# Kernel optimization log

Hardware: AMD Instinct MI355X
Metric: run time of the kernel (lower is better)

## Reference

```python
import jax, jax.numpy as jnp
import numpy as np

BATCH, SEQ, H, P, HID, CHUNK = 2, 2048, 32, 64, 2048, 256
NORM_EPS = 1e-5


def setup_inputs() -> dict:
    key = jax.random.key(0)
    ks = jax.random.split(key, 10)
    f = lambda k, sh, sc=1.0: jax.random.normal(k, sh, jnp.float32) * sc
    return {
        "hidden_states_ab": f(ks[0], (BATCH, SEQ, HID), 0.02),
        "hidden_states_g": f(ks[1], (BATCH, SEQ, HID), 0.02),
        "q_states": f(ks[2], (BATCH, SEQ, H, P)),
        "k_states": f(ks[3], (BATCH, SEQ, H, P)),
        "v_states": f(ks[4], (BATCH, SEQ, H, P)),
        "dt_w": f(ks[5], (HID, H), 0.02),
        "dt_b": jnp.zeros((H,), jnp.float32),
        "g_w": f(ks[6], (HID, H), 0.02),
        "g_b": jnp.zeros((H,), jnp.float32),
        "A_log": jnp.log(jnp.arange(1, H + 1, dtype=jnp.float32)),
        "dt_bias": jnp.ones((H,), jnp.float32),
        "norm_weight": jnp.ones((H * P,), jnp.float32),
        "o_w": f(ks[7], (H, P, P), 0.02),
        "o_b": jnp.zeros((H, P), jnp.float32),
    }


def _l2norm(x, eps=1e-12):
    # torch F.normalize(p=2, dim=-1): x / max(||x||, eps)
    n = jnp.sqrt(jnp.sum(x * x, axis=-1, keepdims=True))
    return x / jnp.maximum(n, eps)


def _ssd(x, dt, A, Bm, Cm, chunk):
    # x: (b,s,h,p)  dt: (b,s,h) post-softplus  A: (h,)  Bm/Cm: (b,s,h,n)
    b, s, h, p = x.shape
    n = Bm.shape[-1]
    c = s // chunk
    rs = lambda t: t.reshape(b, c, chunk, *t.shape[2:])
    x, dt, Bm, Cm = rs(x), rs(dt), rs(Bm), rs(Cm)
    a = dt * A                         # (b,c,L,h) log-decay increments
    cum = jnp.cumsum(a, axis=2)        # (b,c,L,h)
    cumT = jnp.swapaxes(cum, 2, 3)     # (b,c,h,L)
    # intra-chunk (quadratic, causal) part
    diff = cumT[..., :, None] - cumT[..., None, :]          # (b,c,h,L,L)
    mask = jnp.tril(jnp.ones((chunk, chunk), bool))
    decay = jnp.exp(jnp.where(mask, diff, -jnp.inf))
    CB = jnp.einsum('bclhn,bcshn->bchls', Cm, Bm)
    scores = CB * decay * jnp.swapaxes(dt, 2, 3)[:, :, :, None, :]
    y = jnp.einsum('bchls,bcshp->bclhp', scores, x)
    # per-chunk states
    decay_last = jnp.exp(cumT[..., -1:] - cumT)             # (b,c,h,L)
    w = jnp.swapaxes(decay_last, 2, 3) * dt                 # (b,c,L,h)
    states = jnp.einsum('bclh,bclhn,bclhp->bchpn', w, Bm, x)
    # inter-chunk recurrence over c chunks
    chunk_decay = jnp.exp(cumT[..., -1])                    # (b,c,h)
    def step(Hs, inp):
        cd, st = inp
        return cd[..., None, None] * Hs + st, Hs
    H_last, H_prev = jax.lax.scan(
        step, jnp.zeros((b, h, p, n), x.dtype),
        (jnp.moveaxis(chunk_decay, 1, 0), jnp.moveaxis(states, 1, 0)))
    H_prev = jnp.moveaxis(H_prev, 0, 1)                     # (b,c,h,p,n)
    y = y + jnp.einsum('bclhn,bclh,bchpn->bclhp', Cm, jnp.exp(cum), H_prev)
    return y.reshape(b, s, h, p), H_last


def reference(hidden_states_ab, hidden_states_g, q_states, k_states, v_states,
              dt_w, dt_b, g_w, g_b, A_log, dt_bias, norm_weight, o_w, o_b):
    b, s, h, p = v_states.shape
    Cm = _l2norm(q_states)
    Bm = _l2norm(k_states)
    # dt_proj bias + mamba dt_bias, then softplus (dt_softplus=True)
    dt = jax.nn.softplus(hidden_states_ab @ dt_w + dt_b + dt_bias)   # (b,s,h)
    A = -jnp.exp(A_log)
    y, ssm_state = _ssd(v_states, dt, A, Bm, Cm, CHUNK)
    # gate: g_proj then repeat_interleave(head_dim) on last dim
    gate = jnp.repeat(hidden_states_g @ g_w + g_b, p, axis=-1)       # (b,s,h*p)
    # RMSNormGated, norm_before_gate=False: normalize(x * silu(z)) * weight
    y = y.reshape(b, s, h * p) * jax.nn.silu(gate)
    y = y * jax.lax.rsqrt(jnp.mean(y * y, axis=-1, keepdims=True) + NORM_EPS)
    y = y * norm_weight
    # GroupLinear o_proj: per-head (p -> p) linear
    out = jnp.einsum('bshp,hpq->bshq', y.reshape(b, s, h, p), o_w) + o_b
    return out.reshape(b, s, h * p)
```

## Files before the change

### kernel.cpp

```cpp
#include <hip/hip_runtime.h>
#include <math.h>

#define BATCH 2
#define SEQ   2048
#define NH    32
#define HID   2048
#define CHUNK 256
#define NCH   8
#define NBCH  (BATCH*NCH*NH)
#define PST   72
#define BK    256
#define APST  264
#define KSPLIT 4
#define KSEG  (HID / KSPLIT)

typedef __attribute__((ext_vector_type(4))) float f32x4;
typedef __attribute__((ext_vector_type(8))) short bf16x8;
typedef unsigned int uint;
typedef unsigned short ushort;

__device__ __forceinline__ float softplusf(float x) {
    return x > 20.f ? x : log1pf(expf(x));
}

__device__ __forceinline__ short f2bf(float f) {
    union { float f; uint u; } v; v.f = f;
    uint r = v.u + 0x7FFF + ((v.u >> 16) & 1);
    return (short)(r >> 16);
}
__device__ __forceinline__ float bf2f(ushort s) {
    union { uint u; float f; } v; v.u = ((uint)s) << 16; return v.f;
}
__device__ __forceinline__ uint packbf2(float lo, float hi) {
    return (uint)(ushort)f2bf(lo) | ((uint)(ushort)f2bf(hi) << 16);
}

struct BF8 { union { bf16x8 v; short s[8]; }; };

__device__ __forceinline__ bf16x8 load_cvt8(const float* p, float scale) {
    float4 a = *(const float4*)p;
    float4 b = *(const float4*)(p + 4);
    BF8 r;
    r.s[0]=f2bf(a.x*scale); r.s[1]=f2bf(a.y*scale); r.s[2]=f2bf(a.z*scale); r.s[3]=f2bf(a.w*scale);
    r.s[4]=f2bf(b.x*scale); r.s[5]=f2bf(b.y*scale); r.s[6]=f2bf(b.z*scale); r.s[7]=f2bf(b.w*scale);
    return r.v;
}

#define MFMA(a,b,c) __builtin_amdgcn_mfma_f32_16x16x32_bf16((a),(b),(c),0,0,0)

__global__ __launch_bounds__(256) void k_proj(
    const float* __restrict__ hs_ab, const float* __restrict__ hs_g,
    const float* __restrict__ dt_w, const float* __restrict__ g_w,
    float* __restrict__ part)
{
    __shared__ short As[32 * APST];
    __shared__ short Bs[32 * APST];
    int blk = blockIdx.x;
    int ksp = blk >> 8;
    int rem = blk & 255;
    int which = rem >> 7;
    int rt = rem & 127;
    int r0 = rt * 32;
    const float* Am = which ? hs_g : hs_ab;
    const float* W  = which ? g_w  : dt_w;
    int t = threadIdx.x;
    int w = t >> 6, lane = t & 63, quad = lane >> 4, l16 = lane & 15;
    int mh = w & 1, nh = w >> 1;

    f32x4 acc = (f32x4){0.f, 0.f, 0.f, 0.f};

    for (int kc = ksp * KSEG; kc < ksp * KSEG + KSEG; kc += BK) {
        __syncthreads();
        {
            int row = t >> 3, k0 = (t & 7) * 32;
            const float* src = Am + (size_t)(r0 + row) * HID + kc + k0;
            uint* dst = (uint*)(As + row * APST + k0);
            #pragma unroll
            for (int i = 0; i < 4; ++i) {
                float4 a = *(const float4*)(src + i * 8);
                float4 b = *(const float4*)(src + i * 8 + 4);
                dst[i*4+0] = packbf2(a.x, a.y); dst[i*4+1] = packbf2(a.z, a.w);
                dst[i*4+2] = packbf2(b.x, b.y); dst[i*4+3] = packbf2(b.z, b.w);
            }
        }
        if (t < 128) {
            int k2 = t * 2;
            const float* w0 = W + (size_t)(kc + k2) * NH;
            const float* w1 = w0 + NH;
            #pragma unroll
            for (int n = 0; n < 32; n += 4) {
                float4 a = *(const float4*)(w0 + n);
                float4 b = *(const float4*)(w1 + n);
                *((uint*)(Bs + (n+0) * APST + k2)) = packbf2(a.x, b.x);
                *((uint*)(Bs + (n+1) * APST + k2)) = packbf2(a.y, b.y);
                *((uint*)(Bs + (n+2) * APST + k2)) = packbf2(a.z, b.z);
                *((uint*)(Bs + (n+3) * APST + k2)) = packbf2(a.w, b.w);
            }
        }
        __syncthreads();
        #pragma unroll
        for (int ks = 0; ks < BK / 32; ++ks) {
            bf16x8 af = *(const bf16x8*)(As + (mh*16 + l16) * APST + ks*32 + quad*8);
            bf16x8 bf = *(const bf16x8*)(Bs + (nh*16 + l16) * APST + ks*32 + quad*8);
            acc = MFMA(af, bf, acc);
        }
    }

    int n = nh * 16 + l16;
    int Rb = r0 + mh * 16 + quad * 4;
    float* pd = part + ((size_t)(which * KSPLIT + ksp) * 4096 + Rb) * 32 + n;
    #pragma unroll
    for (int r = 0; r < 4; ++r)
        pd[r * 32] = acc[r];
}

__global__ __launch_bounds__(256) void k_proj_fin(
    const float* __restrict__ part,
    const float* __restrict__ dt_b, const float* __restrict__ g_b,
    const float* __restrict__ dt_bias,
    float* __restrict__ dt_out, float* __restrict__ g_out)
{
    int id = blockIdx.x * 256 + threadIdx.x;
    int which = id >> 17;
    int rid = id & 131071;
    int n = rid & 31;
    const float* p = part + (size_t)which * (KSPLIT * 131072) + rid;
    float s = p[0] + p[131072] + p[262144] + p[393216];
    if (which == 0)
        dt_out[rid] = softplusf(s + dt_b[n] + dt_bias[n]);
    else
        g_out[rid] = s + g_b[n];
}

__global__ __launch_bounds__(256) void k_norms(
    const float* __restrict__ q, const float* __restrict__ k,
    float* __restrict__ invC, float* __restrict__ invB)
{
    int t = threadIdx.x;
    int lane = t & 63;
    size_t row = (size_t)blockIdx.x * 4 + (t >> 6);
    float qv = q[row * 64 + lane];
    float kv = k[row * 64 + lane];
    float sq = qv * qv, sk = kv * kv;
    #pragma unroll
    for (int off = 32; off > 0; off >>= 1) {
        sq += __shfl_down(sq, off);
        sk += __shfl_down(sk, off);
    }
    if (lane == 0) {
        invC[row] = 1.f / fmaxf(sqrtf(sq), 1e-12f);
        invB[row] = 1.f / fmaxf(sqrtf(sk), 1e-12f);
    }
}

__global__ __launch_bounds__(256) void k_cumsum(
    const float* __restrict__ dt, const float* __restrict__ A_log,
    float* __restrict__ cumc, float* __restrict__ wvc,
    float* __restrict__ dtc, float* __restrict__ cd)
{
    __shared__ float sC[256];
    int bch = blockIdx.x;
    int h = bch & 31, c = (bch >> 5) & 7, b = bch >> 8;
    int t = threadIdx.x;
    size_t row = ((size_t)b * SEQ + c * CHUNK + t) * NH + h;
    float dt_l = dt[row];
    float A = -expf(A_log[h]);
    sC[t] = dt_l * A;
    __syncthreads();
    for (int off = 1; off < 256; off <<= 1) {
        float v = (t >= off) ? sC[t - off] : 0.f;
        __syncthreads();
        sC[t] += v;
        __syncthreads();
    }
    float cum = sC[t], cl = sC[255];
    size_t o = (size_t)bch * CHUNK + t;
    cumc[o] = cum;
    wvc[o] = expf(cl - cum) * dt_l;
    dtc[o] = dt_l;
    if (t == 255) cd[bch] = expf(cl);
}

__global__ __launch_bounds__(256) void k_states(
    const float* __restrict__ kst, const float* __restrict__ vst,
    const float* __restrict__ invB, const float* __restrict__ wvc,
    float* __restrict__ sp)
{
    __shared__ float kS[64 * 64];
    __shared__ float xS[64 * 64];
    int blk = blockIdx.x;
    int half = blk & 1, bch = blk >> 1;
    int h = bch & 31, c = (bch >> 5) & 7, b = bch >> 8;
    int t = threadIdx.x;
    size_t rowbase = (size_t)b * SEQ + c * CHUNK + half * 128;
    int pg = (t & 15) * 4, ng = (t >> 4) * 4;
    float acc[4][4];
    #pragma unroll
    for (int i = 0; i < 4; ++i)
        #pragma unroll
        for (int j = 0; j < 4; ++j) acc[i][j] = 0.f;

    for (int tt = 0; tt < 2; ++tt) {
        int r0 = t >> 4;
        int c4 = (t & 15) * 4;
        #pragma unroll
        for (int i = 0; i < 4; ++i) {
            int row = r0 + i * 16;
            size_t grow = (rowbase + tt * 64 + row) * NH + h;
            float w  = wvc[(size_t)bch * CHUNK + half * 128 + tt * 64 + row];
            float ib = invB[grow];
            float4 kv = *(const float4*)(kst + grow * 64 + c4);
            float4 xv = *(const float4*)(vst + grow * 64 + c4);
            *(float4*)(kS + row * 64 + c4) =
                make_float4(kv.x * ib, kv.y * ib, kv.z * ib, kv.w * ib);
            *(float4*)(xS + row * 64 + c4) =
                make_float4(xv.x * w, xv.y * w, xv.z * w, xv.w * w);
        }
        __syncthreads();
        for (int ll = 0; ll < 64; ++ll) {
            float4 x4 = *(const float4*)(xS + ll * 64 + pg);
            float4 k4 = *(const float4*)(kS + ll * 64 + ng);
            acc[0][0] += x4.x * k4.x; acc[0][1] += x4.x * k4.y;
            acc[0][2] += x4.x * k4.z; acc[0][3] += x4.x * k4.w;
            acc[1][0] += x4.y * k4.x; acc[1][1] += x4.y * k4.y;
            acc[1][2] += x4.y * k4.z; acc[1][3] += x4.y * k4.w;
            acc[2][0] += x4.z * k4.x; acc[2][1] += x4.z * k4.y;
            acc[2][2] += x4.z * k4.z; acc[2][3] += x4.z * k4.w;
            acc[3][0] += x4.w * k4.x; acc[3][1] += x4.w * k4.y;
            acc[3][2] += x4.w * k4.z; acc[3][3] += x4.w * k4.w;
        }
        __syncthreads();
    }
    size_t obase = (size_t)blk * 4096;
    #pragma unroll
    for (int i = 0; i < 4; ++i)
        *(float4*)(sp + obase + (pg + i) * 64 + ng) =
            make_float4(acc[i][0], acc[i][1], acc[i][2], acc[i][3]);
}

__global__ __launch_bounds__(256) void k_scan(
    const float* __restrict__ sp, const float* __restrict__ cd,
    float* __restrict__ Hp)
{
    size_t id = (size_t)blockIdx.x * 256 + threadIdx.x;
    size_t bh = id >> 12, pn = id & 4095;
    size_t b = bh >> 5, h = bh & 31;
    float carry = 0.f;
    for (int c = 0; c < NCH; ++c) {
        size_t bch = (b * NCH + c) * NH + h;
        float st = sp[(bch * 2) * 4096 + pn] + sp[(bch * 2 + 1) * 4096 + pn];
        Hp[bch * 4096 + pn] = carry;
        carry = cd[bch] * carry + st;
    }
}

__global__ __launch_bounds__(256, 2) void k_intra(
    const float* __restrict__ qst, const float* __restrict__ kst,
    const float* __restrict__ vst,
    const float* __restrict__ invC, const float* __restrict__ invB,
    const float* __restrict__ cumc, const float* __restrict__ dtc,
    const float* __restrict__ Hp,
    short* __restrict__ ygb)
{
    __shared__ short B_s[64 * PST];
    __shared__ short XT_s[64 * PST];
    __shared__ short P_s[4 * 32 * PST];
    __shared__ float sCum[256];
    __shared__ float sDt[256];

    int bch = blockIdx.x;
    int h = bch & 31, c = (bch >> 5) & 7, b = bch >> 8;
    int t = threadIdx.x;
    int w = t >> 6, lane = t & 63;
    int quad = lane >> 4, l16 = lane & 15;
    size_t rowbase = (size_t)b * SEQ + c * CHUNK;

    sCum[t] = cumc[(size_t)bch * CHUNK + t];
    sDt[t]  = dtc[(size_t)bch * CHUNK + t];
    __syncthreads();

    bf16x8 cf[2][2][2];
    #pragma unroll
    for (int is = 0; is < 2; ++is) {
        int strip = is ? (7 - w) : w;
        #pragma unroll
        for (int lt = 0; lt < 2; ++lt) {
            int l = strip * 32 + lt * 16 + l16;
            size_t grow = (rowbase + l) * NH + h;
            float ic = invC[grow];
            const float* qp = qst + grow * 64 + quad * 8;
            cf[is][lt][0] = load_cvt8(qp, ic);
            cf[is][lt][1] = load_cvt8(qp + 32, ic);
        }
    }

    f32x4 acc[2][2][4];
    #pragma unroll
    for (int is = 0; is < 2; ++is)
        #pragma unroll
        for (int lt = 0; lt < 2; ++lt)
            #pragma unroll
            for (int pt = 0; pt < 4; ++pt)
                acc[is][lt][pt] = (f32x4){0.f, 0.f, 0.f, 0.f};

    {
        bf16x8 hf[4][2];
        #pragma unroll
        for (int pt = 0; pt < 4; ++pt) {
            const float* hp = Hp + (size_t)bch * 4096 + (pt * 16 + l16) * 64 + quad * 8;
            hf[pt][0] = load_cvt8(hp, 1.f);
            hf[pt][1] = load_cvt8(hp + 32, 1.f);
        }
        #pragma unroll
        for (int is = 0; is < 2; ++is)
            #pragma unroll
            for (int lt = 0; lt < 2; ++lt)
                #pragma unroll
                for (int pt = 0; pt < 4; ++pt) {
                    acc[is][lt][pt] = MFMA(cf[is][lt][0], hf[pt][0], acc[is][lt][pt]);
                    acc[is][lt][pt] = MFMA(cf[is][lt][1], hf[pt][1], acc[is][lt][pt]);
                }
    }
    #pragma unroll
    for (int is = 0; is < 2; ++is) {
        int strip = is ? (7 - w) : w;
        #pragma unroll
        for (int lt = 0; lt < 2; ++lt) {
            float e[4];
            #pragma unroll
            for (int r = 0; r < 4; ++r)
                e[r] = __expf(sCum[strip * 32 + lt * 16 + quad * 4 + r]);
            #pragma unroll
            for (int pt = 0; pt < 4; ++pt)
                #pragma unroll
                for (int r = 0; r < 4; ++r)
                    acc[is][lt][pt][r] *= e[r];
        }
    }

    short* Pw = P_s + w * 32 * PST;

    for (int st = 0; st < 4; ++st) {
        __syncthreads();
        {
            int ss = t >> 2, q4 = (t & 3) * 16;
            size_t grow = (rowbase + st * 64 + ss) * NH + h;
            float ib = invB[grow];
            const float4* kp = (const float4*)(kst + grow * 64 + q4);
            float4 v0 = kp[0], v1 = kp[1], v2 = kp[2], v3 = kp[3];
            uint u[8];
            u[0] = packbf2(v0.x * ib, v0.y * ib); u[1] = packbf2(v0.z * ib, v0.w * ib);
            u[2] = packbf2(v1.x * ib, v1.y * ib); u[3] = packbf2(v1.z * ib, v1.w * ib);
            u[4] = packbf2(v2.x * ib, v2.y * ib); u[5] = packbf2(v2.z * ib, v2.w * ib);
            u[6] = packbf2(v3.x * ib, v3.y * ib); u[7] = packbf2(v3.z * ib, v3.w * ib);
            uint* dst = (uint*)(B_s + ss * PST + q4);
            *(uint4*)dst = make_uint4(u[0], u[1], u[2], u[3]);
            *(uint4*)(dst + 4) = make_uint4(u[4], u[5], u[6], u[7]);
        }
        {
            int ss2 = t & 31, qh = t >> 5;
            int p0 = qh * 8;
            size_t g0 = (rowbase + st * 64 + 2 * ss2) * NH + h;
            size_t g1 = g0 + NH;
            float dt0 = sDt[st * 64 + 2 * ss2];
            float dt1 = sDt[st * 64 + 2 * ss2 + 1];
            float4 a0 = *(const float4*)(vst + g0 * 64 + p0);
            float4 a1 = *(const float4*)(vst + g0 * 64 + p0 + 4);
            float4 b0 = *(const float4*)(vst + g1 * 64 + p0);
            float4 b1 = *(const float4*)(vst + g1 * 64 + p0 + 4);
            float x0[8] = {a0.x, a0.y, a0.z, a0.w, a1.x, a1.y, a1.z, a1.w};
            float x1[8] = {b0.x, b0.y, b0.z, b0.w, b1.x, b1.y, b1.z, b1.w};
            uint* xt = (uint*)XT_s;
            #pragma unroll
            for (int i = 0; i < 8; ++i)
                xt[(p0 + i) * (PST / 2) + ss2] = packbf2(x0[i] * dt0, x1[i] * dt1);
        }
        __syncthreads();

        bf16x8 xf[4][2];
        #pragma unroll
        for (int pt = 0; pt < 4; ++pt) {
            #pragma unroll
            for (int ks = 0; ks < 2; ++ks)
                xf[pt][ks] = *(const bf16x8*)(XT_s + (pt * 16 + l16) * PST + ks * 32 + quad * 8);
        }

        #pragma unroll
        for (int is = 0; is < 2; ++is) {
            int strip = is ? (7 - w) : w;
            int L0 = strip * 32;
            if (L0 + 31 < st * 64) continue;

            #pragma unroll
            for (int lt = 0; lt < 2; ++lt) {
                int Lt = L0 + lt * 16;
                float cl = sCum[Lt + l16];
                int lrow = lt * 16 + l16;
                #pragma unroll
                for (int mt = 0; mt < 4; ++mt) {
                    int S0 = st * 64 + mt * 16;
                    uint* pdst = (uint*)(Pw + lrow * PST + mt * 16 + quad * 4);
                    if (S0 > Lt + 15) {
                        *(uint2*)pdst = make_uint2(0u, 0u);
                        continue;
                    }
                    f32x4 sa = (f32x4){0.f, 0.f, 0.f, 0.f};
                    bf16x8 af0 = *(const bf16x8*)(B_s + (mt * 16 + l16) * PST + quad * 8);
                    bf16x8 af1 = *(const bf16x8*)(B_s + (mt * 16 + l16) * PST + 32 + quad * 8);
                    sa = MFMA(af0, cf[is][lt][0], sa);
                    sa = MFMA(af1, cf[is][lt][1], sa);
                    float vals[4];
                    #pragma unroll
                    for (int r = 0; r < 4; ++r) {
                        int s = S0 + quad * 4 + r;
                        float v = sa[r] * __expf(cl - sCum[s]);
                        vals[r] = (Lt + l16 >= s) ? v : 0.f;
                    }
                    *(uint2*)pdst = make_uint2(packbf2(vals[0], vals[1]),
                                               packbf2(vals[2], vals[3]));
                }
            }
            #pragma unroll
            for (int lt = 0; lt < 2; ++lt) {
                int Lmax = L0 + lt * 16 + 15;
                #pragma unroll
                for (int ks = 0; ks < 2; ++ks) {
                    if (st * 64 + ks * 32 > Lmax) continue;
                    bf16x8 af = *(const bf16x8*)(Pw + (lt * 16 + l16) * PST + ks * 32 + quad * 8);
                    #pragma unroll
                    for (int pt = 0; pt < 4; ++pt)
                        acc[is][lt][pt] = MFMA(af, xf[pt][ks], acc[is][lt][pt]);
                }
            }
        }
    }

    #pragma unroll
    for (int is = 0; is < 2; ++is) {
        int strip = is ? (7 - w) : w;
        #pragma unroll
        for (int lt = 0; lt < 2; ++lt)
            #pragma unroll
            for (int pt = 0; pt < 4; ++pt)
                #pragma unroll
                for (int r = 0; r < 4; ++r) {
                    int l = strip * 32 + lt * 16 + quad * 4 + r;
                    int p = pt * 16 + l16;
                    ygb[((rowbase + l) * NH + h) * 64 + p] = f2bf(acc[is][lt][pt][r]);
                }
    }
}

__global__ __launch_bounds__(256) void k_gate(
    const short* __restrict__ ygb, const float* __restrict__ g_ws,
    const float* __restrict__ norm_w, short* __restrict__ ygn)
{
    __shared__ float sil[32];
    __shared__ float red[256];
    int r = blockIdx.x;
    int t = threadIdx.x;
    if (t < 32) {
        float g = g_ws[(size_t)r * 32 + t];
        sil[t] = g / (1.f + expf(-g));
    }
    __syncthreads();
    uint4 u = *(const uint4*)(ygb + (size_t)r * 2048 + t * 8);
    float s = sil[t >> 3];
    float v[8];
    v[0] = bf2f(u.x & 0xFFFF) * s; v[1] = bf2f(u.x >> 16) * s;
    v[2] = bf2f(u.y & 0xFFFF) * s; v[3] = bf2f(u.y >> 16) * s;
    v[4] = bf2f(u.z & 0xFFFF) * s; v[5] = bf2f(u.z >> 16) * s;
    v[6] = bf2f(u.w & 0xFFFF) * s; v[7] = bf2f(u.w >> 16) * s;
    float ssq = 0.f;
    #pragma unroll
    for (int i = 0; i < 8; ++i) ssq += v[i] * v[i];
    red[t] = ssq;
    __syncthreads();
    for (int off = 128; off > 0; off >>= 1) {
        if (t < off) red[t] += red[t + off];
        __syncthreads();
    }
    float scale = rsqrtf(red[0] / 2048.f + 1e-5f);
    const float* nw = norm_w + t * 8;
    uint4 o;
    o.x = packbf2(v[0] * scale * nw[0], v[1] * scale * nw[1]);
    o.y = packbf2(v[2] * scale * nw[2], v[3] * scale * nw[3]);
    o.z = packbf2(v[4] * scale * nw[4], v[5] * scale * nw[5]);
    o.w = packbf2(v[6] * scale * nw[6], v[7] * scale * nw[7]);
    *(uint4*)(ygn + (size_t)r * 2048 + t * 8) = o;
}

__global__ __launch_bounds__(256) void k_oproj(
    const short* __restrict__ ygn, const float* __restrict__ o_w,
    const float* __restrict__ o_b, float* __restrict__ out)
{
    __shared__ short wT[64 * PST];
    int blk = blockIdx.x;
    int h = blk & 31, rt = blk >> 5;
    int t = threadIdx.x;
    int w = t >> 6, lane = t & 63;
    int quad = lane >> 4, l16 = lane & 15;

    {
        int p = t >> 2, q4 = (t & 3) * 16;
        const float* wp = o_w + (size_t)h * 4096 + p * 64 + q4;
        float4 v0 = *(const float4*)wp, v1 = *(const float4*)(wp + 4);
        float4 v2 = *(const float4*)(wp + 8), v3 = *(const float4*)(wp + 12);
        float vv[16] = {v0.x,v0.y,v0.z,v0.w, v1.x,v1.y,v1.z,v1.w,
                        v2.x,v2.y,v2.z,v2.w, v3.x,v3.y,v3.z,v3.w};
        #pragma unroll
        for (int i = 0; i < 16; ++i)
            wT[(q4 + i) * PST + p] = f2bf(vv[i]);
    }
    __syncthreads();

    bf16x8 bfr[4][2];
    #pragma unroll
    for (int nt = 0; nt < 4; ++nt)
        #pragma unroll
        for (int ks = 0; ks < 2; ++ks)
            bfr[nt][ks] = *(const bf16x8*)(wT + (nt * 16 + l16) * PST + ks * 32 + quad * 8);

    int rowbase = rt * 256 + w * 64;
    f32x4 acc[4][4];
    #pragma unroll
    for (int nt = 0; nt < 4; ++nt) {
        float bv = o_b[h * 64 + nt * 16 + l16];
        #pragma unroll
        for (int mt = 0; mt < 4; ++mt)
            acc[mt][nt] = (f32x4){bv, bv, bv, bv};
    }
    #pragma unroll
    for (int ks = 0; ks < 2; ++ks) {
        #pragma unroll
        for (int mt = 0; mt < 4; ++mt) {
            int row = rowbase + mt * 16 + l16;
            bf16x8 af = *(const bf16x8*)(ygn + (size_t)row * 2048 + h * 64 + ks * 32 + quad * 8);
            #pragma unroll
            for (int nt = 0; nt < 4; ++nt)
                acc[mt][nt] = MFMA(af, bfr[nt][ks], acc[mt][nt]);
        }
    }
    #pragma unroll
    for (int mt = 0; mt < 4; ++mt)
        #pragma unroll
        for (int nt = 0; nt < 4; ++nt)
            #pragma unroll
            for (int r = 0; r < 4; ++r) {
                int row = rowbase + mt * 16 + quad * 4 + r;
                out[(size_t)row * 2048 + h * 64 + nt * 16 + l16] = acc[mt][nt][r];
            }
}

extern "C" void kernel_launch(void* const* d_in, const int* in_sizes, int n_in,
                              void* d_out, int out_size, void* d_ws, size_t ws_size,
                              hipStream_t stream) {
    const float* hs_ab   = (const float*)d_in[0];
    const float* hs_g    = (const float*)d_in[1];
    const float* qst     = (const float*)d_in[2];
    const float* kst     = (const float*)d_in[3];
    const float* vst     = (const float*)d_in[4];
    const float* dt_w    = (const float*)d_in[5];
    const float* dt_b    = (const float*)d_in[6];
    const float* g_w     = (const float*)d_in[7];
    const float* g_b     = (const float*)d_in[8];
    const float* A_log   = (const float*)d_in[9];
    const float* dt_bias = (const float*)d_in[10];
    const float* norm_w  = (const float*)d_in[11];
    const float* o_w     = (const float*)d_in[12];
    const float* o_b     = (const float*)d_in[13];
    float* out = (float*)d_out;

    float* ws = (float*)d_ws;
    size_t off = 0;
    float* part   = ws + off; off += (size_t)2 * KSPLIT * 4096 * 32;
    float* dt_ws  = ws + off; off += (size_t)BATCH * SEQ * NH;
    float* g_ws   = ws + off; off += (size_t)BATCH * SEQ * NH;
    float* invC   = ws + off; off += (size_t)BATCH * SEQ * NH;
    float* invB   = ws + off; off += (size_t)BATCH * SEQ * NH;
    float* cumc   = ws + off; off += (size_t)NBCH * CHUNK;
    float* wvc    = ws + off; off += (size_t)NBCH * CHUNK;
    float* dtc    = ws + off; off += (size_t)NBCH * CHUNK;
    float* cd_ws  = ws + off; off += (size_t)NBCH;
    float* sp     = ws + off; off += (size_t)NBCH * 2 * 4096;
    float* Hp     = ws + off; off += (size_t)NBCH * 4096;

    short* ygb = (short*)sp;
    short* ygn = (short*)sp + (size_t)BATCH * SEQ * NH * 64;

    k_proj<<<2 * KSPLIT * (BATCH * SEQ / 32), 256, 0, stream>>>(
        hs_ab, hs_g, dt_w, g_w, part);
    k_proj_fin<<<2 * BATCH * SEQ * NH / 256, 256, 0, stream>>>(
        part, dt_b, g_b, dt_bias, dt_ws, g_ws);
    k_norms<<<BATCH * SEQ * NH / 4, 256, 0, stream>>>(qst, kst, invC, invB);
    k_cumsum<<<NBCH, 256, 0, stream>>>(dt_ws, A_log, cumc, wvc, dtc, cd_ws);
    k_states<<<NBCH * 2, 256, 0, stream>>>(kst, vst, invB, wvc, sp);
    k_scan<<<BATCH * NH * 4096 / 256, 256, 0, stream>>>(sp, cd_ws, Hp);
    k_intra<<<NBCH, 256, 0, stream>>>(qst, kst, vst, invC, invB,
                                      cumc, dtc, Hp, ygb);
    k_gate<<<BATCH * SEQ, 256, 0, stream>>>(ygb, g_ws, norm_w, ygn);
    k_oproj<<<32 * (BATCH * SEQ / 256), 256, 0, stream>>>(ygn, o_w, o_b, out);
}
```

Before: 286.7 us.

## Fuse projection finish, l2 norms, gating and o_proj to cut kernel launches

```diff
diff --git a/kernel.cpp b/kernel.cpp
--- a/kernel.cpp
+++ b/kernel.cpp
@@ -46,16 +46,51 @@
     return r.v;
 }
 
+__device__ __forceinline__ bf16x8 cvt8(float4 a, float4 b, float s) {
+    BF8 r;
+    r.s[0]=f2bf(a.x*s); r.s[1]=f2bf(a.y*s); r.s[2]=f2bf(a.z*s); r.s[3]=f2bf(a.w*s);
+    r.s[4]=f2bf(b.x*s); r.s[5]=f2bf(b.y*s); r.s[6]=f2bf(b.z*s); r.s[7]=f2bf(b.w*s);
+    return r.v;
+}
+
 #define MFMA(a,b,c) __builtin_amdgcn_mfma_f32_16x16x32_bf16((a),(b),(c),0,0,0)
 
 __global__ __launch_bounds__(256) void k_proj(
     const float* __restrict__ hs_ab, const float* __restrict__ hs_g,
     const float* __restrict__ dt_w, const float* __restrict__ g_w,
-    float* __restrict__ part)
+    const float* __restrict__ o_w,  const float* __restrict__ norm_w,
+    float* __restrict__ part, short* __restrict__ nwWT)
 {
-    __shared__ short As[32 * APST];
-    __shared__ short Bs[32 * APST];
+    __shared__ __align__(16) short As[32 * APST];
+    __shared__ __align__(16) short Bs[32 * APST];
     int blk = blockIdx.x;
+    int t = threadIdx.x;
+
+    if (blk >= 2 * KSPLIT * 128) {
+        int h = blk - 2 * KSPLIT * 128;
+        float* tile = (float*)As;
+        {
+            int p = t >> 2, q0 = (t & 3) * 16;
+            const float* wp = o_w + (size_t)h * 4096 + p * 64 + q0;
+            #pragma unroll
+            for (int i = 0; i < 4; ++i)
+                *(float4*)(tile + p * 64 + q0 + i * 4) = *(const float4*)(wp + i * 4);
+        }
+        __syncthreads();
+        int q = t >> 2, p0 = (t & 3) * 16;
+        uint us[8];
+        #pragma unroll
+        for (int j = 0; j < 8; ++j) {
+            float lo = tile[(p0 + 2*j    ) * 64 + q] * norm_w[h * 64 + p0 + 2*j];
+            float hi = tile[(p0 + 2*j + 1) * 64 + q] * norm_w[h * 64 + p0 + 2*j + 1];
+            us[j] = packbf2(lo, hi);
+        }
+        uint* dst = (uint*)(nwWT + (size_t)h * 4096 + q * 64 + p0);
+        *(uint4*)dst       = make_uint4(us[0], us[1], us[2], us[3]);
+        *(uint4*)(dst + 4) = make_uint4(us[4], us[5], us[6], us[7]);
+        return;
+    }
+
     int ksp = blk >> 8;
     int rem = blk & 255;
     int which = rem >> 7;
@@ -63,7 +98,6 @@
     int r0 = rt * 32;
     const float* Am = which ? hs_g : hs_ab;
     const float* W  = which ? g_w  : dt_w;
-    int t = threadIdx.x;
     int w = t >> 6, lane = t & 63, quad = lane >> 4, l16 = lane & 15;
     int mh = w & 1, nh = w >> 1;
 
@@ -114,80 +148,48 @@
         pd[r * 32] = acc[r];
 }
 
-__global__ __launch_bounds__(256) void k_proj_fin(
-    const float* __restrict__ part,
-    const float* __restrict__ dt_b, const float* __restrict__ g_b,
-    const float* __restrict__ dt_bias,
-    float* __restrict__ dt_out, float* __restrict__ g_out)
-{
-    int id = blockIdx.x * 256 + threadIdx.x;
-    int which = id >> 17;
-    int rid = id & 131071;
-    int n = rid & 31;
-    const float* p = part + (size_t)which * (KSPLIT * 131072) + rid;
-    float s = p[0] + p[131072] + p[262144] + p[393216];
-    if (which == 0)
-        dt_out[rid] = softplusf(s + dt_b[n] + dt_bias[n]);
-    else
-        g_out[rid] = s + g_b[n];
-}
-
-__global__ __launch_bounds__(256) void k_norms(
-    const float* __restrict__ q, const float* __restrict__ k,
-    float* __restrict__ invC, float* __restrict__ invB)
-{
-    int t = threadIdx.x;
-    int lane = t & 63;
-    size_t row = (size_t)blockIdx.x * 4 + (t >> 6);
-    float qv = q[row * 64 + lane];
-    float kv = k[row * 64 + lane];
-    float sq = qv * qv, sk = kv * kv;
-    #pragma unroll
-    for (int off = 32; off > 0; off >>= 1) {
-        sq += __shfl_down(sq, off);
-        sk += __shfl_down(sk, off);
-    }
-    if (lane == 0) {
-        invC[row] = 1.f / fmaxf(sqrtf(sq), 1e-12f);
-        invB[row] = 1.f / fmaxf(sqrtf(sk), 1e-12f);
-    }
-}
-
 __global__ __launch_bounds__(256) void k_cumsum(
-    const float* __restrict__ dt, const float* __restrict__ A_log,
+    const float* __restrict__ part, const float* __restrict__ dt_b,
+    const float* __restrict__ dt_bias, const float* __restrict__ A_log,
     float* __restrict__ cumc, float* __restrict__ wvc,
     float* __restrict__ dtc, float* __restrict__ cd)
 {
-    __shared__ float sC[256];
+    __shared__ float wsum[4];
     int bch = blockIdx.x;
     int h = bch & 31, c = (bch >> 5) & 7, b = bch >> 8;
     int t = threadIdx.x;
-    size_t row = ((size_t)b * SEQ + c * CHUNK + t) * NH + h;
-    float dt_l = dt[row];
+    int w = t >> 6, lane = t & 63;
+    int rid = (b * SEQ + c * CHUNK + t) * 32 + h;
+    float s = part[rid] + part[131072 + rid] + part[262144 + rid] + part[393216 + rid];
+    float dt_l = softplusf(s + dt_b[h] + dt_bias[h]);
     float A = -expf(A_log[h]);
-    sC[t] = dt_l * A;
+    float v = dt_l * A;
+    #pragma unroll
+    for (int off = 1; off < 64; off <<= 1) {
+        float u = __shfl_up(v, off);
+        if (lane >= off) v += u;
+    }
+    if (lane == 63) wsum[w] = v;
     __syncthreads();
-    for (int off = 1; off < 256; off <<= 1) {
-        float v = (t >= off) ? sC[t - off] : 0.f;
-        __syncthreads();
-        sC[t] += v;
-        __syncthreads();
-    }
-    float cum = sC[t], cl = sC[255];
+    float pre = 0.f;
+    #pragma unroll
+    for (int i = 0; i < 3; ++i)
+        if (i < w) pre += wsum[i];
+    float cum = v + pre;
+    float tot = wsum[0] + wsum[1] + wsum[2] + wsum[3];
     size_t o = (size_t)bch * CHUNK + t;
     cumc[o] = cum;
-    wvc[o] = expf(cl - cum) * dt_l;
+    wvc[o] = expf(tot - cum) * dt_l;
     dtc[o] = dt_l;
-    if (t == 255) cd[bch] = expf(cl);
+    if (t == 255) cd[bch] = expf(tot);
 }
 
 __global__ __launch_bounds__(256) void k_states(
     const float* __restrict__ kst, const float* __restrict__ vst,
-    const float* __restrict__ invB, const float* __restrict__ wvc,
-    float* __restrict__ sp)
+    const float* __restrict__ wvc, float* __restrict__ sp)
 {
-    __shared__ float kS[64 * 64];
-    __shared__ float xS[64 * 64];
+    __shared__ __align__(16) float kS[64 * 64];
+    __shared__ __align__(16) float xS[64 * 64];
     int blk = blockIdx.x;
     int half = blk & 1, bch = blk >> 1;
     int h = bch & 31, c = (bch >> 5) & 7, b = bch >> 8;
@@ -207,14 +209,17 @@
         for (int i = 0; i < 4; ++i) {
             int row = r0 + i * 16;
             size_t grow = (rowbase + tt * 64 + row) * NH + h;
-            float w  = wvc[(size_t)bch * CHUNK + half * 128 + tt * 64 + row];
-            float ib = invB[grow];
+            float wv = wvc[(size_t)bch * CHUNK + half * 128 + tt * 64 + row];
             float4 kv = *(const float4*)(kst + grow * 64 + c4);
             float4 xv = *(const float4*)(vst + grow * 64 + c4);
+            float ssq = kv.x*kv.x + kv.y*kv.y + kv.z*kv.z + kv.w*kv.w;
+            ssq += __shfl_xor(ssq, 1); ssq += __shfl_xor(ssq, 2);
+            ssq += __shfl_xor(ssq, 4); ssq += __shfl_xor(ssq, 8);
+            float ib = 1.f / fmaxf(sqrtf(ssq), 1e-12f);
             *(float4*)(kS + row * 64 + c4) =
                 make_float4(kv.x * ib, kv.y * ib, kv.z * ib, kv.w * ib);
             *(float4*)(xS + row * 64 + c4) =
-                make_float4(xv.x * w, xv.y * w, xv.z * w, xv.w * w);
+                make_float4(xv.x * wv, xv.y * wv, xv.z * wv, xv.w * wv);
         }
         __syncthreads();
         for (int ll = 0; ll < 64; ++ll) {
@@ -257,14 +262,13 @@
 __global__ __launch_bounds__(256, 2) void k_intra(
     const float* __restrict__ qst, const float* __restrict__ kst,
     const float* __restrict__ vst,
-    const float* __restrict__ invC, const float* __restrict__ invB,
     const float* __restrict__ cumc, const float* __restrict__ dtc,
     const float* __restrict__ Hp,
     short* __restrict__ ygb)
 {
-    __shared__ short B_s[64 * PST];
-    __shared__ short XT_s[64 * PST];
-    __shared__ short P_s[4 * 32 * PST];
+    __shared__ __align__(16) short B_s[64 * PST];
+    __shared__ __align__(16) short XT_s[64 * PST];
+    __shared__ __align__(16) short P_s[4 * 32 * PST];
     __shared__ float sCum[256];
     __shared__ float sDt[256];
 
@@ -287,10 +291,20 @@
         for (int lt = 0; lt < 2; ++lt) {
             int l = strip * 32 + lt * 16 + l16;
             size_t grow = (rowbase + l) * NH + h;
-            float ic = invC[grow];
             const float* qp = qst + grow * 64 + quad * 8;
-            cf[is][lt][0] = load_cvt8(qp, ic);
-            cf[is][lt][1] = load_cvt8(qp + 32, ic);
+            float4 a  = *(const float4*)qp;
+            float4 bq = *(const float4*)(qp + 4);
+            float4 c2 = *(const float4*)(qp + 32);
+            float4 d  = *(const float4*)(qp + 36);
+            float ssq = a.x*a.x + a.y*a.y + a.z*a.z + a.w*a.w
+                      + bq.x*bq.x + bq.y*bq.y + bq.z*bq.z + bq.w*bq.w
+                      + c2.x*c2.x + c2.y*c2.y + c2.z*c2.z + c2.w*c2.w
+                      + d.x*d.x + d.y*d.y + d.z*d.z + d.w*d.w;
+            ssq += __shfl_xor(ssq, 16);
+            ssq += __shfl_xor(ssq, 32);
+            float ic = 1.f / fmaxf(sqrtf(ssq), 1e-12f);
+            cf[is][lt][0] = cvt8(a, bq, ic);
+            cf[is][lt][1] = cvt8(c2, d, ic);
         }
     }
 
@@ -345,9 +359,15 @@
         {
             int ss = t >> 2, q4 = (t & 3) * 16;
             size_t grow = (rowbase + st * 64 + ss) * NH + h;
-            float ib = invB[grow];
             const float4* kp = (const float4*)(kst + grow * 64 + q4);
             float4 v0 = kp[0], v1 = kp[1], v2 = kp[2], v3 = kp[3];
+            float ssq = v0.x*v0.x + v0.y*v0.y + v0.z*v0.z + v0.w*v0.w
+                      + v1.x*v1.x + v1.y*v1.y + v1.z*v1.z + v1.w*v1.w
+                      + v2.x*v2.x + v2.y*v2.y + v2.z*v2.z + v2.w*v2.w
+                      + v3.x*v3.x + v3.y*v3.y + v3.z*v3.z + v3.w*v3.w;
+            ssq += __shfl_xor(ssq, 1);
+            ssq += __shfl_xor(ssq, 2);
+            float ib = 1.f / fmaxf(sqrtf(ssq), 1e-12f);
             uint u[8];
             u[0] = packbf2(v0.x * ib, v0.y * ib); u[1] = packbf2(v0.z * ib, v0.w * ib);
             u[2] = packbf2(v1.x * ib, v1.y * ib); u[3] = packbf2(v1.z * ib, v1.w * ib);
@@ -451,105 +471,91 @@
     }
 }
 
-__global__ __launch_bounds__(256) void k_gate(
-    const short* __restrict__ ygb, const float* __restrict__ g_ws,
-    const float* __restrict__ norm_w, short* __restrict__ ygn)
-{
-    __shared__ float sil[32];
-    __shared__ float red[256];
-    int r = blockIdx.x;
-    int t = threadIdx.x;
-    if (t < 32) {
-        float g = g_ws[(size_t)r * 32 + t];
-        sil[t] = g / (1.f + expf(-g));
-    }
-    __syncthreads();
-    uint4 u = *(const uint4*)(ygb + (size_t)r * 2048 + t * 8);
-    float s = sil[t >> 3];
-    float v[8];
-    v[0] = bf2f(u.x & 0xFFFF) * s; v[1] = bf2f(u.x >> 16) * s;
-    v[2] = bf2f(u.y & 0xFFFF) * s; v[3] = bf2f(u.y >> 16) * s;
-    v[4] = bf2f(u.z & 0xFFFF) * s; v[5] = bf2f(u.z >> 16) * s;
-    v[6] = bf2f(u.w & 0xFFFF) * s; v[7] = bf2f(u.w >> 16) * s;
-    float ssq = 0.f;
-    #pragma unroll
-    for (int i = 0; i < 8; ++i) ssq += v[i] * v[i];
-    red[t] = ssq;
-    __syncthreads();
-    for (int off = 128; off > 0; off >>= 1) {
-        if (t < off) red[t] += red[t + off];
-        __syncthreads();
-    }
-    float scale = rsqrtf(red[0] / 2048.f + 1e-5f);
-    const float* nw = norm_w + t * 8;
-    uint4 o;
-    o.x = packbf2(v[0] * scale * nw[0], v[1] * scale * nw[1]);
-    o.y = packbf2(v[2] * scale * nw[2], v[3] * scale * nw[3]);
-    o.z = packbf2(v[4] * scale * nw[4], v[5] * scale * nw[5]);
-    o.w = packbf2(v[6] * scale * nw[6], v[7] * scale * nw[7]);
-    *(uint4*)(ygn + (size_t)r * 2048 + t * 8) = o;
-}
-
-__global__ __launch_bounds__(256) void k_oproj(
-    const short* __restrict__ ygn, const float* __restrict__ o_w,
+__global__ __launch_bounds__(256) void k_out(
+    const short* __restrict__ ygb, const float* __restrict__ part,
+    const float* __restrict__ g_b, const short* __restrict__ nwWT,
     const float* __restrict__ o_b, float* __restrict__ out)
 {
-    __shared__ short wT[64 * PST];
+    __shared__ __align__(16) short yS[16 * 1024];
+    __shared__ float silS[16 * 32];
+    __shared__ float scaleS[16];
     int blk = blockIdx.x;
-    int h = blk & 31, rt = blk >> 5;
+    int half = blk & 1, rt = blk >> 1;
+    int r0 = rt * 16;
     int t = threadIdx.x;
-    int w = t >> 6, lane = t & 63;
-    int quad = lane >> 4, l16 = lane & 15;
-
-    {
-        int p = t >> 2, q4 = (t & 3) * 16;
-        const float* wp = o_w + (size_t)h * 4096 + p * 64 + q4;
-        float4 v0 = *(const float4*)wp, v1 = *(const float4*)(wp + 4);
-        float4 v2 = *(const float4*)(wp + 8), v3 = *(const float4*)(wp + 12);
-        float vv[16] = {v0.x,v0.y,v0.z,v0.w, v1.x,v1.y,v1.z,v1.w,
-                        v2.x,v2.y,v2.z,v2.w, v3.x,v3.y,v3.z,v3.w};
-        #pragma unroll
-        for (int i = 0; i < 16; ++i)
-            wT[(q4 + i) * PST + p] = f2bf(vv[i]);
+    int w = t >> 6, lane = t & 63, quad = lane >> 4, l16 = lane & 15;
+
+    const float* gpart = part + 4 * 131072;
+    #pragma unroll
+    for (int ii = 0; ii < 2; ++ii) {
+        int idx = t + ii * 256;
+        int rr = idx >> 5, hh = idx & 31;
+        int rid = (r0 + rr) * 32 + hh;
+        float g = gpart[rid] + gpart[131072 + rid] + gpart[262144 + rid]
+                + gpart[393216 + rid] + g_b[hh];
+        silS[idx] = g / (1.f + expf(-g));
     }
     __syncthreads();
 
-    bf16x8 bfr[4][2];
-    #pragma unroll
-    for (int nt = 0; nt < 4; ++nt)
+    int r = t >> 4, cl = t & 15;
+    const char* yrow = (const char*)(ygb + (size_t)(r0 + r) * 2048);
+    float ssq = 0.f;
+    #pragma unroll
+    for (int i = 0; i < 16; ++i) {
+        int cb = i * 256 + cl * 16;
+        uint4 u = *(const uint4*)(yrow + cb);
+        float s = silS[r * 32 + (cb >> 7)];
+        float v0 = bf2f((ushort)(u.x & 0xFFFF)) * s, v1 = bf2f((ushort)(u.x >> 16)) * s;
+        float v2 = bf2f((ushort)(u.y & 0xFFFF)) * s, v3 = bf2f((ushort)(u.y >> 16)) * s;
+        float v4 = bf2f((ushort)(u.z & 0xFFFF)) * s, v5 = bf2f((ushort)(u.z >> 16)) * s;
+        float v6 = bf2f((ushort)(u.w & 0xFFFF)) * s, v7 = bf2f((ushort)(u.w >> 16)) * s;
+        ssq += v0*v0 + v1*v1 + v2*v2 + v3*v3 + v4*v4 + v5*v5 + v6*v6 + v7*v7;
+        if ((cb >> 11) == half) {
+            int cbl = cb & 2047;
+            *(uint4*)((char*)yS + r * 2048 + (cbl ^ ((r & 7) << 4))) = u;
+        }
+    }
+    ssq += __shfl_xor(ssq, 1); ssq += __shfl_xor(ssq, 2);
+    ssq += __shfl_xor(ssq, 4); ssq += __shfl_xor(ssq, 8);
+    if (cl == 0) scaleS[r] = rsqrtf(ssq / 2048.f + 1e-5f);
+    __syncthreads();
+
+    #pragma unroll
+    for (int hh = 0; hh < 4; ++hh) {
+        int h = half * 16 + w * 4 + hh;
+        int hl = h & 15;
+        const short* wb = nwWT + (size_t)h * 4096;
+        bf16x8 bfr[4][2];
+        #pragma unroll
+        for (int nt = 0; nt < 4; ++nt)
+            #pragma unroll
+            for (int ks = 0; ks < 2; ++ks)
+                bfr[nt][ks] = *(const bf16x8*)(wb + (nt * 16 + l16) * 64 + ks * 32 + quad * 8);
+        bf16x8 af[2];
+        #pragma unroll
+        for (int ks = 0; ks < 2; ++ks) {
+            int cbl = hl * 128 + ks * 64 + quad * 16;
+            af[ks] = *(const bf16x8*)((const char*)yS + l16 * 2048 + (cbl ^ ((l16 & 7) << 4)));
+        }
+        f32x4 acc[4];
+        #pragma unroll
+        for (int nt = 0; nt < 4; ++nt) acc[nt] = (f32x4){0.f, 0.f, 0.f, 0.f};
         #pragma unroll
         for (int ks = 0; ks < 2; ++ks)
-            bfr[nt][ks] = *(const bf16x8*)(wT + (nt * 16 + l16) * PST + ks * 32 + quad * 8);
-
-    int rowbase = rt * 256 + w * 64;
-    f32x4 acc[4][4];
-    #pragma unroll
-    for (int nt = 0; nt < 4; ++nt) {
-        float bv = o_b[h * 64 + nt * 16 + l16];
-        #pragma unroll
-        for (int mt = 0; mt < 4; ++mt)
-            acc[mt][nt] = (f32x4){bv, bv, bv, bv};
-    }
-    #pragma unroll
-    for (int ks = 0; ks < 2; ++ks) {
-        #pragma unroll
-        for (int mt = 0; mt < 4; ++mt) {
-            int row = rowbase + mt * 16 + l16;
-            bf16x8 af = *(const bf16x8*)(ygn + (size_t)row * 2048 + h * 64 + ks * 32 + quad * 8);
             #pragma unroll
             for (int nt = 0; nt < 4; ++nt)
-                acc[mt][nt] = MFMA(af, bfr[nt][ks], acc[mt][nt]);
-        }
-    }
-    #pragma unroll
-    for (int mt = 0; mt < 4; ++mt)
-        #pragma unroll
-        for (int nt = 0; nt < 4; ++nt)
-            #pragma unroll
-            for (int r = 0; r < 4; ++r) {
-                int row = rowbase + mt * 16 + quad * 4 + r;
-                out[(size_t)row * 2048 + h * 64 + nt * 16 + l16] = acc[mt][nt][r];
+                acc[nt] = MFMA(af[ks], bfr[nt][ks], acc[nt]);
+        #pragma unroll
+        for (int nt = 0; nt < 4; ++nt) {
+            float bv = o_b[h * 64 + nt * 16 + l16];
+            #pragma unroll
+            for (int rr = 0; rr < 4; ++rr) {
+                int row = quad * 4 + rr;
+                float o = acc[nt][rr] * silS[row * 32 + h] * scaleS[row] + bv;
+                out[(size_t)(r0 + row) * 2048 + h * 64 + nt * 16 + l16] = o;
             }
+        }
+    }
 }
 
 extern "C" void kernel_launch(void* const* d_in, const int* in_sizes, int n_in,
@@ -574,30 +580,22 @@
     float* ws = (float*)d_ws;
     size_t off = 0;
     float* part   = ws + off; off += (size_t)2 * KSPLIT * 4096 * 32;
-    float* dt_ws  = ws + off; off += (size_t)BATCH * SEQ * NH;
-    float* g_ws   = ws + off; off += (size_t)BATCH * SEQ * NH;
-    float* invC   = ws + off; off += (size_t)BATCH * SEQ * NH;
-    float* invB   = ws + off; off += (size_t)BATCH * SEQ * NH;
     float* cumc   = ws + off; off += (size_t)NBCH * CHUNK;
     float* wvc    = ws + off; off += (size_t)NBCH * CHUNK;
     float* dtc    = ws + off; off += (size_t)NBCH * CHUNK;
     float* cd_ws  = ws + off; off += (size_t)NBCH;
     float* sp     = ws + off; off += (size_t)NBCH * 2 * 4096;
     float* Hp     = ws + off; off += (size_t)NBCH * 4096;
+    short* nwWT   = (short*)(ws + off); off += (size_t)NH * 64 * 64 / 2;
 
     short* ygb = (short*)sp;
-    short* ygn = (short*)sp + (size_t)BATCH * SEQ * NH * 64;
-
-    k_proj<<<2 * KSPLIT * (BATCH * SEQ / 32), 256, 0, stream>>>(
-        hs_ab, hs_g, dt_w, g_w, part);
-    k_proj_fin<<<2 * BATCH * SEQ * NH / 256, 256, 0, stream>>>(
-        part, dt_b, g_b, dt_bias, dt_ws, g_ws);
-    k_norms<<<BATCH * SEQ * NH / 4, 256, 0, stream>>>(qst, kst, invC, invB);
-    k_cumsum<<<NBCH, 256, 0, stream>>>(dt_ws, A_log, cumc, wvc, dtc, cd_ws);
-    k_states<<<NBCH * 2, 256, 0, stream>>>(kst, vst, invB, wvc, sp);
+
+    k_proj<<<2 * KSPLIT * (BATCH * SEQ / 32) + NH, 256, 0, stream>>>(
+        hs_ab, hs_g, dt_w, g_w, o_w, norm_w, part, nwWT);
+    k_cumsum<<<NBCH, 256, 0, stream>>>(part, dt_b, dt_bias, A_log,
+                                       cumc, wvc, dtc, cd_ws);
+    k_states<<<NBCH * 2, 256, 0, stream>>>(kst, vst, wvc, sp);
     k_scan<<<BATCH * NH * 4096 / 256, 256, 0, stream>>>(sp, cd_ws, Hp);
-    k_intra<<<NBCH, 256, 0, stream>>>(qst, kst, vst, invC, invB,
-                                      cumc, dtc, Hp, ygb);
-    k_gate<<<BATCH * SEQ, 256, 0, stream>>>(ygb, g_ws, norm_w, ygn);
-    k_oproj<<<32 * (BATCH * SEQ / 256), 256, 0, stream>>>(ygn, o_w, o_b, out);
-}
+    k_intra<<<NBCH, 256, 0, stream>>>(qst, kst, vst, cumc, dtc, Hp, ygb);
+    k_out<<<2 * (BATCH * SEQ / 16), 256, 0, stream>>>(ygb, part, g_b, nwWT, o_b, out);
+}
```

Measured after the change: 270.8 us. 1.06x faster.
